# Kernel tuning notes

Measured on AMD Instinct MI355X. Metric: run time of the kernel, lower is better.

Reference implementation:

```python
import jax, jax.numpy as jnp
import numpy as np

EPS = 1e-12  # torch F.normalize eps

def _l2norm(v, axis):
    n = jnp.sqrt(jnp.sum(v * v, axis=axis, keepdims=True))
    return v / jnp.maximum(n, EPS)

def setup_inputs() -> dict:
    key = jax.random.key(0)
    k1, k2, k3 = jax.random.split(key, 3)
    x = jax.random.normal(k1, (32, 512, 30, 40), dtype=jnp.float32)
    conv_w = jax.random.normal(k2, (64, 512), dtype=jnp.float32) * 0.05
    centroids = jax.random.uniform(k3, (64, 512), dtype=jnp.float32)
    return {"x": x, "conv_w": conv_w, "centroids": centroids}

def reference(x, conv_w, centroids):
    N, C, H, W = x.shape
    K = conv_w.shape[0]
    # descriptor-wise L2 normalization over channel dim
    xn = _l2norm(x, axis=1)
    xf = xn.reshape(N, C, H * W)                      # [N, C, HW]
    # 1x1 conv (no bias) -> soft assignment over clusters
    logits = jnp.einsum('kc,nch->nkh', conv_w, xf)     # [N, K, HW]
    a = jax.nn.softmax(logits, axis=1)
    # fused VLAD: sum_hw a*(x - centroid) = (a @ x^T) - centroid * sum_hw a
    vlad = jnp.einsum('nkh,nch->nkc', a, xf) - a.sum(axis=-1)[..., None] * centroids[None]
    vlad = _l2norm(vlad, axis=2)                      # intra-normalization
    v = vlad.reshape(N, K * C)
    return _l2norm(v, axis=1)
```

## Files before the change

### kernel.cpp

```cpp
#include <hip/hip_runtime.h>
#include <hip/hip_bf16.h>
#include <math.h>

#define N_B   32
#define C_DIM 512
#define K_DIM 64
#define HW    1200
#define PTILE 32
#define NPT   38
#define ASLOT 40

typedef __attribute__((ext_vector_type(8))) short bf16x8;
typedef __attribute__((ext_vector_type(4))) float f32x4;

static __device__ inline short f2bf(float f) {
  __hip_bfloat16 h = __float2bfloat16(f);
  union { __hip_bfloat16 b; short s; } u; u.b = h; return u.s;
}

__global__ __launch_bounds__(256) void k1_logits_softmax(
    const float* __restrict__ x, const float* __restrict__ w,
    unsigned short* __restrict__ a_out, float* __restrict__ invnorm_out,
    float* __restrict__ asum_part)
{
  __shared__ bf16x8 wlds[64 * 8];
  __shared__ bf16x8 xlds[32 * 8];
  __shared__ float  slog[64 * 36];
  __shared__ float  sred[8 * 32];
  __shared__ float  pinv[32], pmax[32], psum[32];

  const int tid  = threadIdx.x;
  const int lane = tid & 63;
  const int wv   = tid >> 6;
  const int n    = blockIdx.x / NPT;
  const int tile = blockIdx.x % NPT;
  const int p0   = tile * PTILE;

  const int sp = tid & 31;
  const int sg = tid >> 5;
  const bool spv = (p0 + sp) < HW;

  const int lr = lane & 15;
  const int lg = lane >> 4;

  const float* xb = x + (size_t)n * C_DIM * HW;

  f32x4 acc0 = {0.f, 0.f, 0.f, 0.f};
  f32x4 acc1 = {0.f, 0.f, 0.f, 0.f};
  float ssq = 0.f;

  for (int c0 = 0; c0 < C_DIM; c0 += 64) {
    {
      const int k = tid >> 3, o = tid & 7;
#pragma unroll
      for (int i = 0; i < 2; ++i) {
        const int kk = k + 32 * i;
        const float* wp = w + (size_t)kk * C_DIM + c0 + o * 8;
        float4 w0 = *(const float4*)wp;
        float4 w1 = *(const float4*)(wp + 4);
        bf16x8 v;
        v[0]=f2bf(w0.x); v[1]=f2bf(w0.y); v[2]=f2bf(w0.z); v[3]=f2bf(w0.w);
        v[4]=f2bf(w1.x); v[5]=f2bf(w1.y); v[6]=f2bf(w1.z); v[7]=f2bf(w1.w);
        wlds[kk * 8 + o] = v;
      }
    }
    {
      float f[8];
#pragma unroll
      for (int j = 0; j < 8; ++j) {
        float v = spv ? xb[(size_t)(c0 + sg * 8 + j) * HW + p0 + sp] : 0.f;
        ssq += v * v;
        f[j] = v;
      }
      bf16x8 v;
#pragma unroll
      for (int j = 0; j < 8; ++j) v[j] = f2bf(f[j]);
      xlds[sp * 8 + sg] = v;
    }
    __syncthreads();
    {
      const int kw = wv * 16;
#pragma unroll
      for (int kc = 0; kc < 2; ++kc) {
        bf16x8 af = wlds[(kw + lr) * 8 + kc * 4 + lg];
        bf16x8 b0 = xlds[lr * 8 + kc * 4 + lg];
        bf16x8 b1 = xlds[(16 + lr) * 8 + kc * 4 + lg];
        acc0 = __builtin_amdgcn_mfma_f32_16x16x32_bf16(af, b0, acc0, 0, 0, 0);
        acc1 = __builtin_amdgcn_mfma_f32_16x16x32_bf16(af, b1, acc1, 0, 0, 0);
      }
    }
    __syncthreads();
  }

  sred[sg * 32 + sp] = ssq;
  __syncthreads();
  if (tid < 32) {
    float s = 0.f;
#pragma unroll
    for (int g = 0; g < 8; ++g) s += sred[g * 32 + tid];
    float iv = 1.f / fmaxf(sqrtf(s), 1e-12f);
    pinv[tid] = iv;
    if ((p0 + tid) < HW) invnorm_out[n * HW + p0 + tid] = iv;
  }
  __syncthreads();

  {
    const int kw = wv * 16;
    const float i0 = pinv[lr];
    const float i1 = pinv[16 + lr];
#pragma unroll
    for (int r = 0; r < 4; ++r) {
      slog[(kw + lg * 4 + r) * 36 + lr]      = acc0[r] * i0;
      slog[(kw + lg * 4 + r) * 36 + 16 + lr] = acc1[r] * i1;
    }
  }
  __syncthreads();

  {
    const int p = tid & 31;
    const int kg = tid >> 5;
    float e[8];
    float m = -1e30f;
#pragma unroll
    for (int j = 0; j < 8; ++j) { e[j] = slog[(kg * 8 + j) * 36 + p]; m = fmaxf(m, e[j]); }
    sred[kg * 32 + p] = m;
    __syncthreads();
    if (tid < 32) {
      float mm = sred[tid];
#pragma unroll
      for (int g = 1; g < 8; ++g) mm = fmaxf(mm, sred[g * 32 + tid]);
      pmax[tid] = mm;
    }
    __syncthreads();
    const float M = pmax[p];
    float s = 0.f;
#pragma unroll
    for (int j = 0; j < 8; ++j) { e[j] = __expf(e[j] - M); s += e[j]; }
    sred[kg * 32 + p] = s;
    __syncthreads();
    if (tid < 32) {
      float ss = 0.f;
#pragma unroll
      for (int g = 0; g < 8; ++g) ss += sred[g * 32 + tid];
      psum[tid] = 1.f / ss;
    }
    __syncthreads();
    const float sc = psum[p];
    const bool pv = (p0 + p) < HW;
#pragma unroll
    for (int j = 0; j < 8; ++j) {
      float av = e[j] * sc;
      if (pv) a_out[((size_t)n * K_DIM + kg * 8 + j) * HW + p0 + p] =
                  (unsigned short)f2bf(av);
      float t = pv ? av : 0.f;
#pragma unroll
      for (int off = 16; off > 0; off >>= 1) t += __shfl_xor(t, off);
      if (p == 0) asum_part[((size_t)n * K_DIM + kg * 8 + j) * ASLOT + tile] = t;
    }
  }
}

__global__ __launch_bounds__(256) void k2_vlad_gemm(
    const float* __restrict__ x, const unsigned short* __restrict__ a_in,
    const float* __restrict__ invnorm, float* __restrict__ part)
{
  const int tid  = threadIdx.x;
  const int lane = tid & 63;
  const int wv   = tid >> 6;
  const int b    = blockIdx.x;
  const int half = b & 1;
  const int ct   = (b >> 1) & 7;
  const int n    = b >> 4;
  const int c0   = ct * 64;
  const int hb   = half * 600;
  const int k0   = wv * 16;
  const int lr = lane & 15, lg = lane >> 4;

  const float* xb          = x       + (size_t)n * C_DIM * HW;
  const unsigned short* ab = a_in    + (size_t)n * K_DIM * HW;
  const float* inb         = invnorm + (size_t)n * HW;

  f32x4 acc[4] = {{0,0,0,0}, {0,0,0,0}, {0,0,0,0}, {0,0,0,0}};

  for (int hc = 0; hc < 600; hc += 32) {
    const int hrel = hc + lg * 8;
    const bool gv = hrel < 600;
    const int h = hb + hrel;

    bf16x8 af;
    float4 i0, i1;
    if (gv) {
      af = *(const bf16x8*)(ab + (size_t)(k0 + lr) * HW + h);
      i0 = *(const float4*)(inb + h);
      i1 = *(const float4*)(inb + h + 4);
    } else {
#pragma unroll
      for (int j = 0; j < 8; ++j) af[j] = 0;
      i0 = make_float4(0.f, 0.f, 0.f, 0.f);
      i1 = make_float4(0.f, 0.f, 0.f, 0.f);
    }
#pragma unroll
    for (int cg = 0; cg < 4; ++cg) {
      bf16x8 bx;
      if (gv) {
        const float* xp = xb + (size_t)(c0 + cg * 16 + lr) * HW + h;
        float4 x0 = *(const float4*)xp;
        float4 x1 = *(const float4*)(xp + 4);
        bx[0]=f2bf(x0.x*i0.x); bx[1]=f2bf(x0.y*i0.y);
        bx[2]=f2bf(x0.z*i0.z); bx[3]=f2bf(x0.w*i0.w);
        bx[4]=f2bf(x1.x*i1.x); bx[5]=f2bf(x1.y*i1.y);
        bx[6]=f2bf(x1.z*i1.z); bx[7]=f2bf(x1.w*i1.w);
      } else {
#pragma unroll
        for (int j = 0; j < 8; ++j) bx[j] = 0;
      }
      acc[cg] = __builtin_amdgcn_mfma_f32_16x16x32_bf16(af, bx, acc[cg], 0, 0, 0);
    }
  }

  float* pb = part + (((size_t)half * N_B + n) * K_DIM) * C_DIM;
#pragma unroll
  for (int cg = 0; cg < 4; ++cg)
#pragma unroll
    for (int r = 0; r < 4; ++r)
      pb[(size_t)(k0 + lg * 4 + r) * C_DIM + c0 + cg * 16 + lr] = acc[cg][r];
}

__global__ __launch_bounds__(128) void k3a_intranorm(
    const float* __restrict__ part, const float* __restrict__ cent,
    const float* __restrict__ asum_part, float* __restrict__ out,
    float* __restrict__ rowsum)
{
  const int nk = blockIdx.x;
  const int n = nk >> 6, k = nk & 63;
  const int tid = threadIdx.x;

  __shared__ float sasum;
  __shared__ float wss[2];

  float t = (tid < NPT) ? asum_part[(size_t)nk * ASLOT + tid] : 0.f;
  if (tid < 64) {
#pragma unroll
    for (int off = 32; off > 0; off >>= 1) t += __shfl_xor(t, off);
    if (tid == 0) sasum = t;
  }
  __syncthreads();
  const float asum = sasum;

  const float* p0 = part + ((size_t)n * K_DIM + k) * C_DIM;
  const float* p1 = part + ((size_t)(N_B + n) * K_DIM + k) * C_DIM;
  const float* cb = cent + (size_t)k * C_DIM;

  float4 a4 = *(const float4*)&p0[tid * 4];
  float4 b4 = *(const float4*)&p1[tid * 4];
  float4 c4 = *(const float4*)&cb[tid * 4];
  float4 v;
  v.x = a4.x + b4.x - asum * c4.x;
  v.y = a4.y + b4.y - asum * c4.y;
  v.z = a4.z + b4.z - asum * c4.z;
  v.w = a4.w + b4.w - asum * c4.w;

  float ss = v.x * v.x + v.y * v.y + v.z * v.z + v.w * v.w;
#pragma unroll
  for (int off = 32; off > 0; off >>= 1) ss += __shfl_xor(ss, off);
  if ((tid & 63) == 0) wss[tid >> 6] = ss;
  __syncthreads();
  float tot = wss[0] + wss[1];
  float inv = 1.f / fmaxf(sqrtf(tot), 1e-12f);

  float4 o = make_float4(v.x * inv, v.y * inv, v.z * inv, v.w * inv);
  *(float4*)&out[(size_t)n * (K_DIM * C_DIM) + k * C_DIM + tid * 4] = o;
  if (tid == 0) rowsum[nk] = tot * inv * inv;
}

__global__ __launch_bounds__(256) void k3b_globalnorm(
    const float* __restrict__ rowsum, float* __restrict__ out)
{
  const int b = blockIdx.x;
  const int n = b >> 3, seg = b & 7;
  const int tid = threadIdx.x;

  __shared__ float sg;
  float t = (tid < 64) ? rowsum[n * 64 + tid] : 0.f;
  if (tid < 64) {
#pragma unroll
    for (int off = 32; off > 0; off >>= 1) t += __shfl_xor(t, off);
    if (tid == 0) sg = t;
  }
  __syncthreads();
  float ginv = 1.f / fmaxf(sqrtf(sg), 1e-12f);

  float* ob = out + (size_t)n * (K_DIM * C_DIM) + seg * 4096;
#pragma unroll
  for (int i = 0; i < 4; ++i) {
    float4 v = *(float4*)&ob[(i * 256 + tid) * 4];
    v.x *= ginv; v.y *= ginv; v.z *= ginv; v.w *= ginv;
    *(float4*)&ob[(i * 256 + tid) * 4] = v;
  }
}

extern "C" void kernel_launch(void* const* d_in, const int* in_sizes, int n_in,
                              void* d_out, int out_size, void* d_ws, size_t ws_size,
                              hipStream_t stream) {
  (void)in_sizes; (void)n_in; (void)out_size; (void)ws_size;
  const float* x    = (const float*)d_in[0];
  const float* w    = (const float*)d_in[1];
  const float* cent = (const float*)d_in[2];
  float* out = (float*)d_out;

  char* ws = (char*)d_ws;
  unsigned short* a_buf = (unsigned short*)(ws);
  float* invnorm  = (float*)(ws + 4915200);
  float* asum_p   = (float*)(ws + 5068800);
  float* part     = (float*)(ws + 5396480);
  float* rowsum   = (float*)(ws + 22173696);

  k1_logits_softmax<<<N_B * NPT, 256, 0, stream>>>(x, w, a_buf, invnorm, asum_p);
  k2_vlad_gemm<<<N_B * 16, 256, 0, stream>>>(x, a_buf, invnorm, part);
  k3a_intranorm<<<N_B * K_DIM, 128, 0, stream>>>(part, cent, asum_p, out, rowsum);
  k3b_globalnorm<<<N_B * 8, 256, 0, stream>>>(rowsum, out);
}
```

Measured before the change: 171.4 us.

## Fold per-pixel inverse norm into soft-assignment and shrink VLAD GEMM channel tile

The per-pixel inverse L2 norm is now multiplied into the bf16 soft-assignment stored by the first kernel, so the VLAD GEMM reads raw x without loading invnorm or scaling each element. The asum partials still use the unscaled assignment, which keeps the centroid term correct. The VLAD GEMM now covers 32 channels per block instead of 64 and launches twice as many blocks, with a 2x unrolled loop to add parallelism. The trade-off is that each assignment tile is reloaded by twice as many blocks, and rounding the scaled product to bf16 changes precision slightly.

Result: faster. 167.5 us (-2.3%).

```diff
diff --git a/kernel.cpp b/kernel.cpp
--- a/kernel.cpp
+++ b/kernel.cpp
@@ -20,8 +20,7 @@
 
 __global__ __launch_bounds__(256) void k1_logits_softmax(
     const float* __restrict__ x, const float* __restrict__ w,
-    unsigned short* __restrict__ a_out, float* __restrict__ invnorm_out,
-    float* __restrict__ asum_part)
+    unsigned short* __restrict__ a_out, float* __restrict__ asum_part)
 {
   __shared__ bf16x8 wlds[64 * 8];
   __shared__ bf16x8 xlds[32 * 8];
@@ -98,9 +97,7 @@
     float s = 0.f;
 #pragma unroll
     for (int g = 0; g < 8; ++g) s += sred[g * 32 + tid];
-    float iv = 1.f / fmaxf(sqrtf(s), 1e-12f);
-    pinv[tid] = iv;
-    if ((p0 + tid) < HW) invnorm_out[n * HW + p0 + tid] = iv;
+    pinv[tid] = 1.f / fmaxf(sqrtf(s), 1e-12f);
   }
   __syncthreads();
 
@@ -146,84 +143,80 @@
     }
     __syncthreads();
     const float sc = psum[p];
+    const float iv = pinv[p];
     const bool pv = (p0 + p) < HW;
 #pragma unroll
     for (int j = 0; j < 8; ++j) {
       float av = e[j] * sc;
-      if (pv) a_out[((size_t)n * K_DIM + kg * 8 + j) * HW + p0 + p] =
-                  (unsigned short)f2bf(av);
       float t = pv ? av : 0.f;
 #pragma unroll
       for (int off = 16; off > 0; off >>= 1) t += __shfl_xor(t, off);
       if (p == 0) asum_part[((size_t)n * K_DIM + kg * 8 + j) * ASLOT + tile] = t;
+      if (pv) a_out[((size_t)n * K_DIM + kg * 8 + j) * HW + p0 + p] =
+                  (unsigned short)f2bf(av * iv);
     }
   }
 }
 
 __global__ __launch_bounds__(256) void k2_vlad_gemm(
     const float* __restrict__ x, const unsigned short* __restrict__ a_in,
-    const float* __restrict__ invnorm, float* __restrict__ part)
+    float* __restrict__ part)
 {
   const int tid  = threadIdx.x;
   const int lane = tid & 63;
   const int wv   = tid >> 6;
   const int b    = blockIdx.x;
   const int half = b & 1;
-  const int ct   = (b >> 1) & 7;
-  const int n    = b >> 4;
-  const int c0   = ct * 64;
+  const int ct   = (b >> 1) & 15;
+  const int n    = b >> 5;
+  const int c0   = ct * 32;
   const int hb   = half * 600;
   const int k0   = wv * 16;
   const int lr = lane & 15, lg = lane >> 4;
 
-  const float* xb          = x       + (size_t)n * C_DIM * HW;
-  const unsigned short* ab = a_in    + (size_t)n * K_DIM * HW;
-  const float* inb         = invnorm + (size_t)n * HW;
-
-  f32x4 acc[4] = {{0,0,0,0}, {0,0,0,0}, {0,0,0,0}, {0,0,0,0}};
-
+  const float* xb          = x    + (size_t)n * C_DIM * HW;
+  const unsigned short* ab = a_in + (size_t)n * K_DIM * HW;
+
+  f32x4 acc0 = {0,0,0,0}, acc1 = {0,0,0,0};
+
+#pragma unroll 2
   for (int hc = 0; hc < 600; hc += 32) {
     const int hrel = hc + lg * 8;
     const bool gv = hrel < 600;
     const int h = hb + hrel;
 
     bf16x8 af;
-    float4 i0, i1;
+    bf16x8 bx0, bx1;
     if (gv) {
       af = *(const bf16x8*)(ab + (size_t)(k0 + lr) * HW + h);
-      i0 = *(const float4*)(inb + h);
-      i1 = *(const float4*)(inb + h + 4);
-    } else {
-#pragma unroll
-      for (int j = 0; j < 8; ++j) af[j] = 0;
-      i0 = make_float4(0.f, 0.f, 0.f, 0.f);
-      i1 = make_float4(0.f, 0.f, 0.f, 0.f);
-    }
-#pragma unroll
-    for (int cg = 0; cg < 4; ++cg) {
-      bf16x8 bx;
-      if (gv) {
-        const float* xp = xb + (size_t)(c0 + cg * 16 + lr) * HW + h;
+      {
+        const float* xp = xb + (size_t)(c0 + lr) * HW + h;
         float4 x0 = *(const float4*)xp;
         float4 x1 = *(const float4*)(xp + 4);
-        bx[0]=f2bf(x0.x*i0.x); bx[1]=f2bf(x0.y*i0.y);
-        bx[2]=f2bf(x0.z*i0.z); bx[3]=f2bf(x0.w*i0.w);
-        bx[4]=f2bf(x1.x*i1.x); bx[5]=f2bf(x1.y*i1.y);
-        bx[6]=f2bf(x1.z*i1.z); bx[7]=f2bf(x1.w*i1.w);
-      } else {
-#pragma unroll
-        for (int j = 0; j < 8; ++j) bx[j] = 0;
-      }
-      acc[cg] = __builtin_amdgcn_mfma_f32_16x16x32_bf16(af, bx, acc[cg], 0, 0, 0);
-    }
+        bx0[0]=f2bf(x0.x); bx0[1]=f2bf(x0.y); bx0[2]=f2bf(x0.z); bx0[3]=f2bf(x0.w);
+        bx0[4]=f2bf(x1.x); bx0[5]=f2bf(x1.y); bx0[6]=f2bf(x1.z); bx0[7]=f2bf(x1.w);
+      }
+      {
+        const float* xp = xb + (size_t)(c0 + 16 + lr) * HW + h;
+        float4 x0 = *(const float4*)xp;
+        float4 x1 = *(const float4*)(xp + 4);
+        bx1[0]=f2bf(x0.x); bx1[1]=f2bf(x0.y); bx1[2]=f2bf(x0.z); bx1[3]=f2bf(x0.w);
+        bx1[4]=f2bf(x1.x); bx1[5]=f2bf(x1.y); bx1[6]=f2bf(x1.z); bx1[7]=f2bf(x1.w);
+      }
+    } else {
+#pragma unroll
+      for (int j = 0; j < 8; ++j) { af[j] = 0; bx0[j] = 0; bx1[j] = 0; }
+    }
+    acc0 = __builtin_amdgcn_mfma_f32_16x16x32_bf16(af, bx0, acc0, 0, 0, 0);
+    acc1 = __builtin_amdgcn_mfma_f32_16x16x32_bf16(af, bx1, acc1, 0, 0, 0);
   }
 
   float* pb = part + (((size_t)half * N_B + n) * K_DIM) * C_DIM;
 #pragma unroll
-  for (int cg = 0; cg < 4; ++cg)
-#pragma unroll
-    for (int r = 0; r < 4; ++r)
-      pb[(size_t)(k0 + lg * 4 + r) * C_DIM + c0 + cg * 16 + lr] = acc[cg][r];
+  for (int r = 0; r < 4; ++r) {
+    pb[(size_t)(k0 + lg * 4 + r) * C_DIM + c0 + lr]      = acc0[r];
+    pb[(size_t)(k0 + lg * 4 + r) * C_DIM + c0 + 16 + lr] = acc1[r];
+  }
 }
 
 __global__ __launch_bounds__(128) void k3a_intranorm(
@@ -310,13 +303,12 @@
 
   char* ws = (char*)d_ws;
   unsigned short* a_buf = (unsigned short*)(ws);
-  float* invnorm  = (float*)(ws + 4915200);
-  float* asum_p   = (float*)(ws + 5068800);
-  float* part     = (float*)(ws + 5396480);
-  float* rowsum   = (float*)(ws + 22173696);
-
-  k1_logits_softmax<<<N_B * NPT, 256, 0, stream>>>(x, w, a_buf, invnorm, asum_p);
-  k2_vlad_gemm<<<N_B * 16, 256, 0, stream>>>(x, a_buf, invnorm, part);
+  float* asum_p   = (float*)(ws + 4915200);
+  float* part     = (float*)(ws + 5242880);
+  float* rowsum   = (float*)(ws + 22020096);
+
+  k1_logits_softmax<<<N_B * NPT, 256, 0, stream>>>(x, w, a_buf, asum_p);
+  k2_vlad_gemm<<<N_B * 32, 256, 0, stream>>>(x, a_buf, part);
   k3a_intranorm<<<N_B * K_DIM, 128, 0, stream>>>(part, cent, asum_p, out, rowsum);
   k3b_globalnorm<<<N_B * 8, 256, 0, stream>>>(rowsum, out);
 }
```
